# Performance work log

Measured on AMD Instinct MI355X. Metric: run time of the kernel, lower is better.

Reference implementation:

```python
import jax, jax.numpy as jnp
import numpy as np

B, W, F_IN = 128, 128, 64   # batch, window_size, num_features
N = 64                      # nodes per graph == num_features == tcn_out_channels
E = 4096                    # edges per graph
ED = 16                     # edge_feature_dim
H, C = 4, 32                # heads, gat_out_dim
FLAT = N * H * C            # 8192
HID = FLAT // 4             # 2048
LRELU_SLOPE = 0.01          # F.leaky_relu default
BN_EPS = 1e-5


def setup_inputs() -> dict:
    key = jax.random.key(0)
    ks = jax.random.split(key, 16)
    x = jax.random.normal(ks[0], (B, W, F_IN), jnp.float32)
    edge_index = jax.random.randint(ks[1], (2, E), 0, N)
    edge_attr = jax.random.normal(ks[2], (B, E, ED), jnp.float32)
    s = lambda k, shape, fan: jax.random.normal(k, shape, jnp.float32) / np.sqrt(fan)
    tcn_w = s(ks[3], (N, F_IN, 3), F_IN * 3)
    tcn_b = jnp.zeros((N,), jnp.float32)
    lin_l_w = s(ks[4], (H * C, W), W)
    lin_l_b = jnp.zeros((H * C,), jnp.float32)
    lin_e_w = s(ks[5], (H * C, ED), ED)
    lin_e_b = jnp.zeros((H * C,), jnp.float32)
    att = s(ks[6], (1, H, C), C)
    fc1_w = s(ks[7], (HID, FLAT), FLAT)
    fc1_b = jnp.zeros((HID,), jnp.float32)
    bn_g = jnp.ones((HID,), jnp.float32)
    bn_b = jnp.zeros((HID,), jnp.float32)
    fc2_w = s(ks[8], (2, HID), HID)
    fc2_b = jnp.zeros((2,), jnp.float32)
    return dict(x=x, edge_index=edge_index, edge_attr=edge_attr,
                tcn_w=tcn_w, tcn_b=tcn_b,
                lin_l_w=lin_l_w, lin_l_b=lin_l_b,
                lin_e_w=lin_e_w, lin_e_b=lin_e_b, att=att,
                fc1_w=fc1_w, fc1_b=fc1_b, bn_g=bn_g, bn_b=bn_b,
                fc2_w=fc2_w, fc2_b=fc2_b)


def reference(x, edge_index, edge_attr, tcn_w, tcn_b,
              lin_l_w, lin_l_b, lin_e_w, lin_e_b, att,
              fc1_w, fc1_b, bn_g, bn_b, fc2_w, fc2_b):
    # TCN: Conv1d(k=3, pad=1) over the window dim
    xt = jnp.transpose(x, (0, 2, 1))  # [B, F_IN, W]
    x_g = jax.lax.conv_general_dilated(
        xt, tcn_w, window_strides=(1,), padding=((1, 1),),
        dimension_numbers=('NCH', 'OIH', 'NCH')) + tcn_b[None, :, None]
    # x_g: [B, N, W] -> per-sample graph with N nodes, W-dim node features

    src, dst = edge_index[0], edge_index[1]

    def gat_one(xn, ea):
        # xn: [N, W], ea: [E, ED]
        h = (xn @ lin_l_w.T + lin_l_b).reshape(N, H, C)
        e = (ea @ lin_e_w.T + lin_e_b).reshape(E, H, C)
        xi = h[dst]               # [E, H, C] target node feats
        xj = h[src]               # [E, H, C] source node feats
        a = jax.nn.leaky_relu(xi + xj + e, LRELU_SLOPE)
        score = jnp.einsum('ehc,ohc->eh', a, att)  # [E, H]
        # segment softmax over edges grouped by destination node
        m = jax.ops.segment_max(score, dst, num_segments=N)
        m = jnp.where(jnp.isfinite(m), m, 0.0)
        ex = jnp.exp(score - m[dst])
        den = jax.ops.segment_sum(ex, dst, num_segments=N)
        alpha = ex / (den[dst] + 1e-16)            # [E, H]
        msg = xj * alpha[:, :, None]               # [E, H, C]
        out = jax.ops.segment_sum(msg, dst, num_segments=N)  # [N, H, C]
        return out.reshape(N, H * C)

    x_gat = jax.vmap(gat_one)(x_g, edge_attr)      # [B, N, H*C]
    x_gat = jax.nn.elu(x_gat)
    x_flat = x_gat.reshape(B, FLAT)

    h1 = x_flat @ fc1_w.T + fc1_b
    # BatchNorm1d in eval mode with fresh running stats (mean=0, var=1)
    h1 = h1 * (bn_g / jnp.sqrt(1.0 + BN_EPS)) + bn_b
    h1 = jax.nn.relu(h1)  # dropout is identity in eval
    logits = h1 @ fc2_w.T + fc2_b
    return logits
```

## Files before the change

### kernel.cpp

```cpp
#include <hip/hip_runtime.h>
#include <math.h>

#define BB   128
#define WW   128
#define FIN  64
#define NNODE 64
#define NE   4096
#define EDIM 16
#define NH   4
#define CDIM 32
#define HC   128
#define FLATD 8192
#define HIDD 2048

#define OFF_H    0u
#define OFF_P    1048576u
#define OFF_XGB  3211264u
#define OFF_BK   4259840u

typedef unsigned short u16;
typedef u16    u16x8  __attribute__((ext_vector_type(8)));
typedef u16    u16x4  __attribute__((ext_vector_type(4)));
typedef __bf16 bf16x8 __attribute__((ext_vector_type(8)));
typedef float  f32x4  __attribute__((ext_vector_type(4)));
typedef float  f32x16 __attribute__((ext_vector_type(16)));

__device__ __forceinline__ u16 f2bf(float f) {
    unsigned u = __float_as_uint(f);
    u += 0x7fffu + ((u >> 16) & 1u);
    return (u16)(u >> 16);
}
__device__ __forceinline__ void hilo(float v, u16* h, u16* l) {
    u16 hh = f2bf(v);
    float hf = __uint_as_float(((unsigned)hh) << 16);
    *h = hh;
    *l = f2bf(v - hf);
}

__global__ __launch_bounds__(256) void k0_bucket(
        const int* __restrict__ ei, int* __restrict__ bstart, int* __restrict__ blist)
{
    __shared__ int cnt[64];
    __shared__ int cur[65];
    const int t = threadIdx.x;
    if (t < 64) cnt[t] = 0;
    __syncthreads();
    for (int e = t; e < NE; e += 256) atomicAdd(&cnt[ei[NE + e]], 1);
    __syncthreads();
    if (t == 0) {
        int run = 0;
        for (int n = 0; n < 64; ++n) { cur[n] = run; run += cnt[n]; }
        cur[64] = run;
    }
    __syncthreads();
    if (t < 65) bstart[t] = cur[t];
    __syncthreads();
    for (int e = t; e < NE; e += 256) {
        int d = ei[NE + e], s = ei[e];
        int p = atomicAdd(&cur[d], 1);
        blist[p] = (e << 12) | (d << 6) | s;
    }
}

__global__ __launch_bounds__(256) void k1_tcn_linl(
        const float* __restrict__ x, const float* __restrict__ tcn_w,
        const float* __restrict__ tcn_b, const float* __restrict__ lin_l_w,
        const float* __restrict__ lin_l_b, float* __restrict__ h)
{
    __shared__ float xs[130*65];
    __shared__ float xg[32*132];
    const int b = blockIdx.x, half = blockIdx.y, t = threadIdx.x;
    const int n0 = half * 32;

    for (int idx = t; idx < 8192; idx += 256) {
        int w = idx >> 6, i = idx & 63;
        xs[(w+1)*65 + i] = x[b*8192 + idx];
    }
    if (t < 65) { xs[t] = 0.f; xs[129*65 + t] = 0.f; }
    __syncthreads();

    {
        const int nl = t >> 3;
        const int n  = n0 + nl;
        const int w0 = (t & 7) * 16;
        float acc[16];
        const float tb = tcn_b[n];
#pragma unroll
        for (int j = 0; j < 16; ++j) acc[j] = tb;
        for (int i = 0; i < 64; ++i) {
            const float t0 = tcn_w[n*192 + 3*i + 0];
            const float t1 = tcn_w[n*192 + 3*i + 1];
            const float t2 = tcn_w[n*192 + 3*i + 2];
            float a = xs[(w0+0)*65 + i];
            float c0 = xs[(w0+1)*65 + i];
#pragma unroll
            for (int dw = 0; dw < 16; ++dw) {
                float c = xs[(w0+dw+2)*65 + i];
                acc[dw] += a*t0 + c0*t1 + c*t2;
                a = c0; c0 = c;
            }
        }
#pragma unroll
        for (int dw = 0; dw < 16; ++dw) xg[nl*132 + w0 + dw] = acc[dw];
    }
    __syncthreads();

    {
        const int o2 = t & 63, ng = t >> 6;
        const int oA = o2, oB = o2 + 64;
        float accA[8], accB[8];
        const float lbA = lin_l_b[oA], lbB = lin_l_b[oB];
#pragma unroll
        for (int j = 0; j < 8; ++j) { accA[j] = lbA; accB[j] = lbB; }
        for (int c = 0; c < 32; ++c) {
            const float4 lwA = *(const float4*)&lin_l_w[oA*128 + c*4];
            const float4 lwB = *(const float4*)&lin_l_w[oB*128 + c*4];
#pragma unroll
            for (int nn = 0; nn < 8; ++nn) {
                const float4 xv = *(const float4*)&xg[(ng*8+nn)*132 + c*4];
                accA[nn] += xv.x*lwA.x + xv.y*lwA.y + xv.z*lwA.z + xv.w*lwA.w;
                accB[nn] += xv.x*lwB.x + xv.y*lwB.y + xv.z*lwB.z + xv.w*lwB.w;
            }
        }
#pragma unroll
        for (int nn = 0; nn < 8; ++nn) {
            const int n = n0 + ng*8 + nn;
            h[(b*64 + n)*128 + oA] = accA[nn];
            h[(b*64 + n)*128 + oB] = accB[nn];
        }
    }
}

#define CAPF 1600
__global__ __launch_bounds__(512, 2) void k2_fused(
        const float* __restrict__ hbase, const float* __restrict__ ea,
        const float* __restrict__ lin_e_w, const float* __restrict__ lin_e_b,
        const float* __restrict__ att, const int* __restrict__ bstart,
        const int* __restrict__ blist, u16* __restrict__ xgb)
{
    __shared__ float hbuf[64*132];
    __shared__ float scl[CAPF*4];
    __shared__ float Pm[4][16][68];
    __shared__ int   bst[17];
    const int b = blockIdx.x, quart = blockIdx.y, t = threadIdx.x;
    const int lane = t & 63, wv = t >> 6, l32 = lane & 31, h5 = lane >> 5;

    for (int idx = t; idx < 2048; idx += 512) {
        const int row = idx >> 5, c4 = (idx & 31) * 4;
        float4 hv = *(const float4*)&hbase[(size_t)b*8192 + row*128 + c4];
        const float4 eb = *(const float4*)&lin_e_b[c4];
        hv.x += 0.5f*eb.x; hv.y += 0.5f*eb.y;
        hv.z += 0.5f*eb.z; hv.w += 0.5f*eb.w;
        *(float4*)&hbuf[row*132 + c4] = hv;
    }
    {
        const f32x4 z4 = {0.f, 0.f, 0.f, 0.f};
        for (int idx = t; idx < 4*16*68/4; idx += 512) ((f32x4*)Pm)[idx] = z4;
    }
    if (t < 17) bst[t] = bstart[quart*16 + t];
    bf16x8 Ah[4], Al[4];
#pragma unroll
    for (int mt = 0; mt < 4; ++mt) {
        const float* wp = &lin_e_w[(mt*32 + l32)*16 + h5*8];
        const float4 w0 = *(const float4*)wp;
        const float4 w1 = *(const float4*)(wp + 4);
        u16 th[8], tl[8];
        hilo(w0.x,&th[0],&tl[0]); hilo(w0.y,&th[1],&tl[1]);
        hilo(w0.z,&th[2],&tl[2]); hilo(w0.w,&th[3],&tl[3]);
        hilo(w1.x,&th[4],&tl[4]); hilo(w1.y,&th[5],&tl[5]);
        hilo(w1.z,&th[6],&tl[6]); hilo(w1.w,&th[7],&tl[7]);
        u16x8 vh = { th[0],th[1],th[2],th[3],th[4],th[5],th[6],th[7] };
        u16x8 vl = { tl[0],tl[1],tl[2],tl[3],tl[4],tl[5],tl[6],tl[7] };
        Ah[mt] = *(bf16x8*)&vh;
        Al[mt] = *(bf16x8*)&vl;
    }
    float4 attv[4][4];
#pragma unroll
    for (int mt = 0; mt < 4; ++mt)
#pragma unroll
        for (int g = 0; g < 4; ++g)
            attv[mt][g] = *(const float4*)&att[mt*32 + g*8 + h5*4];
    __syncthreads();

    const int lo = bst[0], cnt = min(bst[16] - lo, CAPF);
    const int gcnt = (cnt + 31) >> 5;

    for (int g = wv; g < gcnt; g += 8) {
        const int idx = g*32 + l32;
        const bool valid = idx < cnt;
        const int pk = valid ? blist[lo + idx] : 0;
        const int sn = pk & 63, dd = (pk >> 6) & 63, e = pk >> 12;
        const float* eap = ea + ((size_t)b*NE + e)*16 + h5*8;
        const float4 v0 = *(const float4*)eap;
        const float4 v1 = *(const float4*)(eap + 4);
        u16 bh[8], bl[8];
        hilo(v0.x,&bh[0],&bl[0]); hilo(v0.y,&bh[1],&bl[1]);
        hilo(v0.z,&bh[2],&bl[2]); hilo(v0.w,&bh[3],&bl[3]);
        hilo(v1.x,&bh[4],&bl[4]); hilo(v1.y,&bh[5],&bl[5]);
        hilo(v1.z,&bh[6],&bl[6]); hilo(v1.w,&bh[7],&bl[7]);
        u16x8 vbh = { bh[0],bh[1],bh[2],bh[3],bh[4],bh[5],bh[6],bh[7] };
        u16x8 vbl = { bl[0],bl[1],bl[2],bl[3],bl[4],bl[5],bl[6],bl[7] };
        const bf16x8 Bh = *(bf16x8*)&vbh;
        const bf16x8 Bl = *(bf16x8*)&vbl;
        float hacc[4];
#pragma unroll
        for (int mt = 0; mt < 4; ++mt) {
            f32x16 D = {0.f,0.f,0.f,0.f,0.f,0.f,0.f,0.f,
                        0.f,0.f,0.f,0.f,0.f,0.f,0.f,0.f};
            D = __builtin_amdgcn_mfma_f32_32x32x16_bf16(Al[mt], Bh, D, 0, 0, 0);
            D = __builtin_amdgcn_mfma_f32_32x32x16_bf16(Ah[mt], Bl, D, 0, 0, 0);
            D = __builtin_amdgcn_mfma_f32_32x32x16_bf16(Ah[mt], Bh, D, 0, 0, 0);
            float s = 0.f;
#pragma unroll
            for (int g4 = 0; g4 < 4; ++g4) {
                const int ob = mt*32 + g4*8 + h5*4;
                const float4 hd = *(const float4*)&hbuf[dd*132 + ob];
                const float4 hs = *(const float4*)&hbuf[sn*132 + ob];
                float x0 = hd.x + hs.x + D[g4*4+0];
                float x1 = hd.y + hs.y + D[g4*4+1];
                float x2 = hd.z + hs.z + D[g4*4+2];
                float x3 = hd.w + hs.w + D[g4*4+3];
                x0 = fmaxf(x0, 0.01f*x0); x1 = fmaxf(x1, 0.01f*x1);
                x2 = fmaxf(x2, 0.01f*x2); x3 = fmaxf(x3, 0.01f*x3);
                const float4 a4 = attv[mt][g4];
                s += a4.x*x0 + a4.y*x1 + a4.z*x2 + a4.w*x3;
            }
            hacc[mt] = s;
        }
#pragma unroll
        for (int hh = 0; hh < 4; ++hh)
            hacc[hh] += __shfl_xor(hacc[hh], 32);
        if (h5 == 0 && valid)
            *(float4*)&scl[idx*4] = make_float4(hacc[0], hacc[1], hacc[2], hacc[3]);
    }
    __syncthreads();

    {
        const int pair = t >> 3, sub = t & 7;
        const int nl = pair >> 2, hh = pair & 3;
        const int s0 = bst[nl] - lo, s1 = bst[nl+1] - lo;
        float mx = -3.4e38f;
        for (int i = s0 + sub; i < s1; i += 8) mx = fmaxf(mx, scl[i*4 + hh]);
        mx = fmaxf(mx, __shfl_xor(mx, 1));
        mx = fmaxf(mx, __shfl_xor(mx, 2));
        mx = fmaxf(mx, __shfl_xor(mx, 4));
        float den = 0.f;
        for (int i = s0 + sub; i < s1; i += 8) {
            const float ex = __expf(scl[i*4 + hh] - mx);
            scl[i*4 + hh] = ex;
            den += ex;
        }
        den += __shfl_xor(den, 1);
        den += __shfl_xor(den, 2);
        den += __shfl_xor(den, 4);
        const float rd = 1.0f / (den + 1e-16f);
        for (int i = s0 + sub; i < s1; i += 8) {
            const int src = blist[lo + i] & 63;
            atomicAdd(&Pm[hh][nl][src], scl[i*4 + hh] * rd);
        }
    }
    __syncthreads();

    {
        const int hh = wv >> 1, ct = wv & 1;
        const int l16 = lane & 15, q = lane >> 4;
        const int cb = hh*32 + ct*16 + l16;
        f32x4 D = {0.f, 0.f, 0.f, 0.f};
#pragma unroll
        for (int k0 = 0; k0 < 64; k0 += 32) {
            const float* pp = &Pm[hh][l16][k0 + q*8];
            const float4 a0 = *(const float4*)pp;
            const float4 a1 = *(const float4*)(pp + 4);
            u16 ph[8], pl[8];
            hilo(a0.x,&ph[0],&pl[0]); hilo(a0.y,&ph[1],&pl[1]);
            hilo(a0.z,&ph[2],&pl[2]); hilo(a0.w,&ph[3],&pl[3]);
            hilo(a1.x,&ph[4],&pl[4]); hilo(a1.y,&ph[5],&pl[5]);
            hilo(a1.z,&ph[6],&pl[6]); hilo(a1.w,&ph[7],&pl[7]);
            u16x8 vph = { ph[0],ph[1],ph[2],ph[3],ph[4],ph[5],ph[6],ph[7] };
            u16x8 vpl = { pl[0],pl[1],pl[2],pl[3],pl[4],pl[5],pl[6],pl[7] };
            u16 hhv[8], hlv[8];
#pragma unroll
            for (int i = 0; i < 8; ++i) {
                const float v = hbuf[(k0 + q*8 + i)*132 + cb];
                hilo(v, &hhv[i], &hlv[i]);
            }
            u16x8 vhh = { hhv[0],hhv[1],hhv[2],hhv[3],hhv[4],hhv[5],hhv[6],hhv[7] };
            u16x8 vhl = { hlv[0],hlv[1],hlv[2],hlv[3],hlv[4],hlv[5],hlv[6],hlv[7] };
            const bf16x8 Ph = *(bf16x8*)&vph, Pl = *(bf16x8*)&vpl;
            const bf16x8 Hh = *(bf16x8*)&vhh, Hl = *(bf16x8*)&vhl;
            D = __builtin_amdgcn_mfma_f32_16x16x32_bf16(Pl, Hh, D, 0, 0, 0);
            D = __builtin_amdgcn_mfma_f32_16x16x32_bf16(Ph, Hl, D, 0, 0, 0);
            D = __builtin_amdgcn_mfma_f32_16x16x32_bf16(Ph, Hh, D, 0, 0, 0);
        }
        const float lb2 = 0.5f * lin_e_b[cb];
#pragma unroll
        for (int r = 0; r < 4; ++r) {
            const int m = q*4 + r;
            const float corr = (bst[m+1] > bst[m]) ? lb2 : 0.f;
            float v = D[r] - corr;
            v = v > 0.f ? v : expm1f(v);
            xgb[(size_t)b*8192 + (quart*16 + m)*128 + cb] = f2bf(v);
        }
    }
}

__global__ __launch_bounds__(256) void k3_fc1(
        const u16* __restrict__ xgb, const float* __restrict__ fc1_w,
        float* __restrict__ part)
{
    __shared__ u16 Ash[128*72];
    __shared__ u16 Bsh[32*72];
    const int jb = blockIdx.x, ks = blockIdx.y, t = threadIdx.x;
    const int j0 = jb*32, k0 = ks*1024;
    const int wave = t >> 6, lane = t & 63;
    const int quad = lane >> 4, l16 = lane & 15;
    const int wm = (wave & 1) * 64, wn = (wave >> 1) * 16;

    f32x4 acc[4];
#pragma unroll
    for (int i = 0; i < 4; ++i) acc[i] = (f32x4){0.f, 0.f, 0.f, 0.f};

    const int arow = t >> 1, acol = (t & 1) * 32;
    const int brow = t >> 3, bcol = (t & 7) * 8;

    for (int kc = 0; kc < 1024; kc += 64) {
        if (kc) __syncthreads();
        const u16* ap = xgb + (size_t)arow*FLATD + k0 + kc + acol;
#pragma unroll
        for (int qq = 0; qq < 4; ++qq)
            *(u16x8*)&Ash[arow*72 + acol + qq*8] = *(const u16x8*)(ap + qq*8);
        const float* bp = fc1_w + (size_t)(j0 + brow)*FLATD + k0 + kc + bcol;
        {
            float4 v0 = *(const float4*)(bp);
            float4 v1 = *(const float4*)(bp + 4);
            u16x8 u = { f2bf(v0.x), f2bf(v0.y), f2bf(v0.z), f2bf(v0.w),
                        f2bf(v1.x), f2bf(v1.y), f2bf(v1.z), f2bf(v1.w) };
            *(u16x8*)&Bsh[brow*72 + bcol] = u;
        }
        __syncthreads();
#pragma unroll
        for (int kk = 0; kk < 64; kk += 32) {
            bf16x8 af[4], bfr;
#pragma unroll
            for (int i = 0; i < 4; ++i)
                af[i] = *(const bf16x8*)&Ash[(wm + i*16 + l16)*72 + kk + quad*8];
            bfr = *(const bf16x8*)&Bsh[(wn + l16)*72 + kk + quad*8];
#pragma unroll
            for (int i = 0; i < 4; ++i)
                acc[i] = __builtin_amdgcn_mfma_f32_16x16x32_bf16(af[i], bfr, acc[i], 0, 0, 0);
        }
    }
#pragma unroll
    for (int i = 0; i < 4; ++i) {
        const int n = j0 + wn + l16;
#pragma unroll
        for (int r = 0; r < 4; ++r) {
            const int m = wm + i*16 + quad*4 + r;
            part[(size_t)ks*262144 + (size_t)m*HIDD + n] = acc[i][r];
        }
    }
}

__global__ __launch_bounds__(256) void k4_fc2(
        const float* __restrict__ part, const float* __restrict__ fc1_b,
        const float* __restrict__ bn_g, const float* __restrict__ bn_b,
        const float* __restrict__ fc2_w, const float* __restrict__ fc2_b,
        float* __restrict__ out)
{
    __shared__ float r0[256], r1[256];
    const int b = blockIdx.x, t = threadIdx.x;
    const float inv = 1.0f / sqrtf(1.0f + 1e-5f);
    float p0 = 0.f, p1 = 0.f;
    for (int j = t; j < 2048; j += 256) {
        float hv = 0.f;
#pragma unroll
        for (int s = 0; s < 8; ++s) hv += part[(size_t)s*262144 + (size_t)b*2048 + j];
        float v = (hv + fc1_b[j]) * (bn_g[j] * inv) + bn_b[j];
        v = fmaxf(v, 0.f);
        p0 += v * fc2_w[j];
        p1 += v * fc2_w[2048 + j];
    }
    r0[t] = p0; r1[t] = p1;
    __syncthreads();
    for (int s = 128; s > 0; s >>= 1) {
        if (t < s) { r0[t] += r0[t+s]; r1[t] += r1[t+s]; }
        __syncthreads();
    }
    if (t == 0) {
        out[b*2 + 0] = r0[0] + fc2_b[0];
        out[b*2 + 1] = r1[0] + fc2_b[1];
    }
}

extern "C" void kernel_launch(void* const* d_in, const int* in_sizes, int n_in,
                              void* d_out, int out_size, void* d_ws, size_t ws_size,
                              hipStream_t stream)
{
    const float* x       = (const float*)d_in[0];
    const int*   ei      = (const int*)  d_in[1];
    const float* ea      = (const float*)d_in[2];
    const float* tcn_w   = (const float*)d_in[3];
    const float* tcn_b   = (const float*)d_in[4];
    const float* lin_l_w = (const float*)d_in[5];
    const float* lin_l_b = (const float*)d_in[6];
    const float* lin_e_w = (const float*)d_in[7];
    const float* lin_e_b = (const float*)d_in[8];
    const float* att     = (const float*)d_in[9];
    const float* fc1_w   = (const float*)d_in[10];
    const float* fc1_b   = (const float*)d_in[11];
    const float* bn_g    = (const float*)d_in[12];
    const float* bn_b    = (const float*)d_in[13];
    const float* fc2_w   = (const float*)d_in[14];
    const float* fc2_b   = (const float*)d_in[15];

    float* ws     = (float*)d_ws;
    float* hbuf   = ws + OFF_H;
    float* part   = ws + OFF_P;
    u16*   xgb    = (u16*)(ws + OFF_XGB);
    int*   bstart = (int*)(ws + OFF_BK);
    int*   blist  = bstart + 80;
    float* out    = (float*)d_out;

    k0_bucket  <<<1, 256, 0, stream>>>(ei, bstart, blist);
    k1_tcn_linl<<<dim3(BB, 2), 256, 0, stream>>>(x, tcn_w, tcn_b, lin_l_w, lin_l_b, hbuf);
    k2_fused   <<<dim3(BB, 4), 512, 0, stream>>>(hbuf, ea, lin_e_w, lin_e_b, att,
                                                 bstart, blist, xgb);
    k3_fc1     <<<dim3(64, 8), 256, 0, stream>>>(xgb, fc1_w, part);
    k4_fc2     <<<BB, 256, 0, stream>>>(part, fc1_b, bn_g, bn_b, fc2_w, fc2_b, out);
}
```

Measured before the change: 252.1 us.

## Merge bucket and TCN kernels, halve GAT split, prefetch edge and fc1 loads

The bucketing kernel is folded into the TCN/lin_l launch as an extra block, and the TCN weights are staged in shared memory. The GAT kernel now handles 32 destination nodes per block instead of 16, with a larger edge-score buffer and occupancy dropped to one block per CU. It also software-prefetches the next edge group's index and features, and reuses the H fragments across two M tiles. The fc1 GEMM register-prefetches the next K slice before the MFMA loop. Together these aim to cut launch count and hide global-load latency, at the cost of fewer, larger GAT blocks (256 total) and more shared-memory pressure.

```diff
diff --git a/kernel.cpp b/kernel.cpp
--- a/kernel.cpp
+++ b/kernel.cpp
@@ -37,44 +37,52 @@
     *l = f2bf(v - hf);
 }
 
-__global__ __launch_bounds__(256) void k0_bucket(
-        const int* __restrict__ ei, int* __restrict__ bstart, int* __restrict__ blist)
-{
-    __shared__ int cnt[64];
-    __shared__ int cur[65];
-    const int t = threadIdx.x;
-    if (t < 64) cnt[t] = 0;
-    __syncthreads();
-    for (int e = t; e < NE; e += 256) atomicAdd(&cnt[ei[NE + e]], 1);
-    __syncthreads();
-    if (t == 0) {
-        int run = 0;
-        for (int n = 0; n < 64; ++n) { cur[n] = run; run += cnt[n]; }
-        cur[64] = run;
-    }
-    __syncthreads();
-    if (t < 65) bstart[t] = cur[t];
-    __syncthreads();
-    for (int e = t; e < NE; e += 256) {
-        int d = ei[NE + e], s = ei[e];
-        int p = atomicAdd(&cur[d], 1);
-        blist[p] = (e << 12) | (d << 6) | s;
-    }
-}
-
-__global__ __launch_bounds__(256) void k1_tcn_linl(
+__global__ __launch_bounds__(256) void k01(
         const float* __restrict__ x, const float* __restrict__ tcn_w,
         const float* __restrict__ tcn_b, const float* __restrict__ lin_l_w,
-        const float* __restrict__ lin_l_b, float* __restrict__ h)
+        const float* __restrict__ lin_l_b, float* __restrict__ h,
+        const int* __restrict__ ei, int* __restrict__ bstart,
+        int* __restrict__ blist)
 {
     __shared__ float xs[130*65];
     __shared__ float xg[32*132];
-    const int b = blockIdx.x, half = blockIdx.y, t = threadIdx.x;
+    __shared__ float tw[32*192];
+    __shared__ int cnt[64];
+    __shared__ int cur[65];
+    const int bid = blockIdx.x, t = threadIdx.x;
+
+    if (bid == 256) {
+        if (t < 64) cnt[t] = 0;
+        __syncthreads();
+        for (int e = t; e < NE; e += 256) atomicAdd(&cnt[ei[NE + e]], 1);
+        __syncthreads();
+        if (t == 0) {
+            int run = 0;
+            for (int n = 0; n < 64; ++n) { cur[n] = run; run += cnt[n]; }
+            cur[64] = run;
+        }
+        __syncthreads();
+        if (t < 65) bstart[t] = cur[t];
+        __syncthreads();
+        for (int e = t; e < NE; e += 256) {
+            int d = ei[NE + e], s = ei[e];
+            int p = atomicAdd(&cur[d], 1);
+            blist[p] = (e << 12) | (d << 6) | s;
+        }
+        return;
+    }
+
+    const int b = bid >> 1, half = bid & 1;
     const int n0 = half * 32;
 
     for (int idx = t; idx < 8192; idx += 256) {
         int w = idx >> 6, i = idx & 63;
         xs[(w+1)*65 + i] = x[b*8192 + idx];
+    }
+    {
+        const float4* src = (const float4*)(tcn_w + n0*192);
+        for (int idx = t; idx < 1536; idx += 256)
+            ((float4*)tw)[idx] = src[idx];
     }
     if (t < 65) { xs[t] = 0.f; xs[129*65 + t] = 0.f; }
     __syncthreads();
@@ -88,9 +96,9 @@
 #pragma unroll
         for (int j = 0; j < 16; ++j) acc[j] = tb;
         for (int i = 0; i < 64; ++i) {
-            const float t0 = tcn_w[n*192 + 3*i + 0];
-            const float t1 = tcn_w[n*192 + 3*i + 1];
-            const float t2 = tcn_w[n*192 + 3*i + 2];
+            const float t0 = tw[nl*192 + 3*i + 0];
+            const float t1 = tw[nl*192 + 3*i + 1];
+            const float t2 = tw[nl*192 + 3*i + 2];
             float a = xs[(w0+0)*65 + i];
             float c0 = xs[(w0+1)*65 + i];
 #pragma unroll
@@ -131,8 +139,8 @@
     }
 }
 
-#define CAPF 1600
-__global__ __launch_bounds__(512, 2) void k2_fused(
+#define CAPF 2560
+__global__ __launch_bounds__(512, 1) void k2_fused(
         const float* __restrict__ hbase, const float* __restrict__ ea,
         const float* __restrict__ lin_e_w, const float* __restrict__ lin_e_b,
         const float* __restrict__ att, const int* __restrict__ bstart,
@@ -140,10 +148,26 @@
 {
     __shared__ float hbuf[64*132];
     __shared__ float scl[CAPF*4];
-    __shared__ float Pm[4][16][68];
-    __shared__ int   bst[17];
-    const int b = blockIdx.x, quart = blockIdx.y, t = threadIdx.x;
+    __shared__ float Pm[4][32][68];
+    __shared__ int   bst[33];
+    const int b = blockIdx.x, half = blockIdx.y, t = threadIdx.x;
     const int lane = t & 63, wv = t >> 6, l32 = lane & 31, h5 = lane >> 5;
+
+    const int lo  = bstart[half*32];
+    const int cnt = min(bstart[half*32 + 32] - lo, CAPF);
+    const int gcnt = (cnt + 31) >> 5;
+
+    int g = wv;
+    int pkc = 0; bool validc = false;
+    float4 v0c = {0.f,0.f,0.f,0.f}, v1c = {0.f,0.f,0.f,0.f};
+    if (g < gcnt) {
+        const int idx0 = g*32 + l32;
+        validc = idx0 < cnt;
+        pkc = validc ? blist[lo + idx0] : 0;
+        const float* eap = ea + ((size_t)b*NE + (size_t)(pkc >> 12))*16 + h5*8;
+        v0c = *(const float4*)eap;
+        v1c = *(const float4*)(eap + 4);
+    }
 
     for (int idx = t; idx < 2048; idx += 512) {
         const int row = idx >> 5, c4 = (idx & 31) * 4;
@@ -155,9 +179,9 @@
     }
     {
         const f32x4 z4 = {0.f, 0.f, 0.f, 0.f};
-        for (int idx = t; idx < 4*16*68/4; idx += 512) ((f32x4*)Pm)[idx] = z4;
-    }
-    if (t < 17) bst[t] = bstart[quart*16 + t];
+        for (int idx = t; idx < 4*32*68/4; idx += 512) ((f32x4*)Pm)[idx] = z4;
+    }
+    if (t < 33) bst[t] = bstart[half*32 + t];
     bf16x8 Ah[4], Al[4];
 #pragma unroll
     for (int mt = 0; mt < 4; ++mt) {
@@ -178,21 +202,26 @@
 #pragma unroll
     for (int mt = 0; mt < 4; ++mt)
 #pragma unroll
-        for (int g = 0; g < 4; ++g)
-            attv[mt][g] = *(const float4*)&att[mt*32 + g*8 + h5*4];
-    __syncthreads();
-
-    const int lo = bst[0], cnt = min(bst[16] - lo, CAPF);
-    const int gcnt = (cnt + 31) >> 5;
-
-    for (int g = wv; g < gcnt; g += 8) {
+        for (int gq = 0; gq < 4; ++gq)
+            attv[mt][gq] = *(const float4*)&att[mt*32 + gq*8 + h5*4];
+    __syncthreads();
+
+    while (g < gcnt) {
+        const int gn = g + 8;
+        const int pk = pkc; const bool valid = validc;
+        const float4 v0 = v0c, v1 = v1c;
         const int idx = g*32 + l32;
-        const bool valid = idx < cnt;
-        const int pk = valid ? blist[lo + idx] : 0;
-        const int sn = pk & 63, dd = (pk >> 6) & 63, e = pk >> 12;
-        const float* eap = ea + ((size_t)b*NE + e)*16 + h5*8;
-        const float4 v0 = *(const float4*)eap;
-        const float4 v1 = *(const float4*)(eap + 4);
+        if (gn < gcnt) {
+            const int idxn = gn*32 + l32;
+            validc = idxn < cnt;
+            pkc = validc ? blist[lo + idxn] : 0;
+            const float* eap = ea + ((size_t)b*NE + (size_t)(pkc >> 12))*16 + h5*8;
+            v0c = *(const float4*)eap;
+            v1c = *(const float4*)(eap + 4);
+        } else {
+            validc = false;
+        }
+        const int sn = pk & 63, dd = (pk >> 6) & 63;
         u16 bh[8], bl[8];
         hilo(v0.x,&bh[0],&bl[0]); hilo(v0.y,&bh[1],&bl[1]);
         hilo(v0.z,&bh[2],&bl[2]); hilo(v0.w,&bh[3],&bl[3]);
@@ -232,29 +261,28 @@
             hacc[hh] += __shfl_xor(hacc[hh], 32);
         if (h5 == 0 && valid)
             *(float4*)&scl[idx*4] = make_float4(hacc[0], hacc[1], hacc[2], hacc[3]);
-    }
-    __syncthreads();
-
-    {
-        const int pair = t >> 3, sub = t & 7;
+        g = gn;
+    }
+    __syncthreads();
+
+    {
+        const int pair = t >> 2, sub = t & 3;
         const int nl = pair >> 2, hh = pair & 3;
         const int s0 = bst[nl] - lo, s1 = bst[nl+1] - lo;
         float mx = -3.4e38f;
-        for (int i = s0 + sub; i < s1; i += 8) mx = fmaxf(mx, scl[i*4 + hh]);
+        for (int i = s0 + sub; i < s1; i += 4) mx = fmaxf(mx, scl[i*4 + hh]);
         mx = fmaxf(mx, __shfl_xor(mx, 1));
         mx = fmaxf(mx, __shfl_xor(mx, 2));
-        mx = fmaxf(mx, __shfl_xor(mx, 4));
         float den = 0.f;
-        for (int i = s0 + sub; i < s1; i += 8) {
+        for (int i = s0 + sub; i < s1; i += 4) {
             const float ex = __expf(scl[i*4 + hh] - mx);
             scl[i*4 + hh] = ex;
             den += ex;
         }
         den += __shfl_xor(den, 1);
         den += __shfl_xor(den, 2);
-        den += __shfl_xor(den, 4);
         const float rd = 1.0f / (den + 1e-16f);
-        for (int i = s0 + sub; i < s1; i += 8) {
+        for (int i = s0 + sub; i < s1; i += 4) {
             const int src = blist[lo + i] & 63;
             atomicAdd(&Pm[hh][nl][src], scl[i*4 + hh] * rd);
         }
@@ -265,41 +293,49 @@
         const int hh = wv >> 1, ct = wv & 1;
         const int l16 = lane & 15, q = lane >> 4;
         const int cb = hh*32 + ct*16 + l16;
-        f32x4 D = {0.f, 0.f, 0.f, 0.f};
-#pragma unroll
-        for (int k0 = 0; k0 < 64; k0 += 32) {
-            const float* pp = &Pm[hh][l16][k0 + q*8];
-            const float4 a0 = *(const float4*)pp;
-            const float4 a1 = *(const float4*)(pp + 4);
-            u16 ph[8], pl[8];
-            hilo(a0.x,&ph[0],&pl[0]); hilo(a0.y,&ph[1],&pl[1]);
-            hilo(a0.z,&ph[2],&pl[2]); hilo(a0.w,&ph[3],&pl[3]);
-            hilo(a1.x,&ph[4],&pl[4]); hilo(a1.y,&ph[5],&pl[5]);
-            hilo(a1.z,&ph[6],&pl[6]); hilo(a1.w,&ph[7],&pl[7]);
-            u16x8 vph = { ph[0],ph[1],ph[2],ph[3],ph[4],ph[5],ph[6],ph[7] };
-            u16x8 vpl = { pl[0],pl[1],pl[2],pl[3],pl[4],pl[5],pl[6],pl[7] };
+        const float lb2 = 0.5f * lin_e_b[cb];
+        bf16x8 Hh2[2], Hl2[2];
+#pragma unroll
+        for (int kk = 0; kk < 2; ++kk) {
             u16 hhv[8], hlv[8];
 #pragma unroll
             for (int i = 0; i < 8; ++i) {
-                const float v = hbuf[(k0 + q*8 + i)*132 + cb];
+                const float v = hbuf[(kk*32 + q*8 + i)*132 + cb];
                 hilo(v, &hhv[i], &hlv[i]);
             }
             u16x8 vhh = { hhv[0],hhv[1],hhv[2],hhv[3],hhv[4],hhv[5],hhv[6],hhv[7] };
             u16x8 vhl = { hlv[0],hlv[1],hlv[2],hlv[3],hlv[4],hlv[5],hlv[6],hlv[7] };
-            const bf16x8 Ph = *(bf16x8*)&vph, Pl = *(bf16x8*)&vpl;
-            const bf16x8 Hh = *(bf16x8*)&vhh, Hl = *(bf16x8*)&vhl;
-            D = __builtin_amdgcn_mfma_f32_16x16x32_bf16(Pl, Hh, D, 0, 0, 0);
-            D = __builtin_amdgcn_mfma_f32_16x16x32_bf16(Ph, Hl, D, 0, 0, 0);
-            D = __builtin_amdgcn_mfma_f32_16x16x32_bf16(Ph, Hh, D, 0, 0, 0);
-        }
-        const float lb2 = 0.5f * lin_e_b[cb];
-#pragma unroll
-        for (int r = 0; r < 4; ++r) {
-            const int m = q*4 + r;
-            const float corr = (bst[m+1] > bst[m]) ? lb2 : 0.f;
-            float v = D[r] - corr;
-            v = v > 0.f ? v : expm1f(v);
-            xgb[(size_t)b*8192 + (quart*16 + m)*128 + cb] = f2bf(v);
+            Hh2[kk] = *(bf16x8*)&vhh;
+            Hl2[kk] = *(bf16x8*)&vhl;
+        }
+#pragma unroll
+        for (int mrow = 0; mrow < 32; mrow += 16) {
+            f32x4 D = {0.f, 0.f, 0.f, 0.f};
+#pragma unroll
+            for (int kk = 0; kk < 2; ++kk) {
+                const float* pp = &Pm[hh][mrow + l16][kk*32 + q*8];
+                const float4 a0 = *(const float4*)pp;
+                const float4 a1 = *(const float4*)(pp + 4);
+                u16 ph[8], pl[8];
+                hilo(a0.x,&ph[0],&pl[0]); hilo(a0.y,&ph[1],&pl[1]);
+                hilo(a0.z,&ph[2],&pl[2]); hilo(a0.w,&ph[3],&pl[3]);
+                hilo(a1.x,&ph[4],&pl[4]); hilo(a1.y,&ph[5],&pl[5]);
+                hilo(a1.z,&ph[6],&pl[6]); hilo(a1.w,&ph[7],&pl[7]);
+                u16x8 vph = { ph[0],ph[1],ph[2],ph[3],ph[4],ph[5],ph[6],ph[7] };
+                u16x8 vpl = { pl[0],pl[1],pl[2],pl[3],pl[4],pl[5],pl[6],pl[7] };
+                const bf16x8 Ph = *(bf16x8*)&vph, Pl = *(bf16x8*)&vpl;
+                D = __builtin_amdgcn_mfma_f32_16x16x32_bf16(Pl, Hh2[kk], D, 0, 0, 0);
+                D = __builtin_amdgcn_mfma_f32_16x16x32_bf16(Ph, Hl2[kk], D, 0, 0, 0);
+                D = __builtin_amdgcn_mfma_f32_16x16x32_bf16(Ph, Hh2[kk], D, 0, 0, 0);
+            }
+#pragma unroll
+            for (int r = 0; r < 4; ++r) {
+                const int m = mrow + q*4 + r;
+                const float corr = (bst[m+1] > bst[m]) ? lb2 : 0.f;
+                float v = D[r] - corr;
+                v = v > 0.f ? v : expm1f(v);
+                xgb[(size_t)b*8192 + (half*32 + m)*128 + cb] = f2bf(v);
+            }
         }
     }
 }
@@ -323,21 +359,32 @@
     const int arow = t >> 1, acol = (t & 1) * 32;
     const int brow = t >> 3, bcol = (t & 7) * 8;
 
+    u16x8 Ar[4]; float4 Br0, Br1;
+    {
+        const u16* ap = xgb + (size_t)arow*FLATD + k0 + acol;
+#pragma unroll
+        for (int qq = 0; qq < 4; ++qq) Ar[qq] = *(const u16x8*)(ap + qq*8);
+        const float* bp = fc1_w + (size_t)(j0 + brow)*FLATD + k0 + bcol;
+        Br0 = *(const float4*)bp; Br1 = *(const float4*)(bp + 4);
+    }
+
     for (int kc = 0; kc < 1024; kc += 64) {
-        if (kc) __syncthreads();
-        const u16* ap = xgb + (size_t)arow*FLATD + k0 + kc + acol;
 #pragma unroll
         for (int qq = 0; qq < 4; ++qq)
-            *(u16x8*)&Ash[arow*72 + acol + qq*8] = *(const u16x8*)(ap + qq*8);
-        const float* bp = fc1_w + (size_t)(j0 + brow)*FLATD + k0 + kc + bcol;
+            *(u16x8*)&Ash[arow*72 + acol + qq*8] = Ar[qq];
         {
-            float4 v0 = *(const float4*)(bp);
-            float4 v1 = *(const float4*)(bp + 4);
-            u16x8 u = { f2bf(v0.x), f2bf(v0.y), f2bf(v0.z), f2bf(v0.w),
-                        f2bf(v1.x), f2bf(v1.y), f2bf(v1.z), f2bf(v1.w) };
+            u16x8 u = { f2bf(Br0.x), f2bf(Br0.y), f2bf(Br0.z), f2bf(Br0.w),
+                        f2bf(Br1.x), f2bf(Br1.y), f2bf(Br1.z), f2bf(Br1.w) };
             *(u16x8*)&Bsh[brow*72 + bcol] = u;
         }
         __syncthreads();
+        if (kc + 64 < 1024) {
+            const u16* ap = xgb + (size_t)arow*FLATD + k0 + kc + 64 + acol;
+#pragma unroll
+            for (int qq = 0; qq < 4; ++qq) Ar[qq] = *(const u16x8*)(ap + qq*8);
+            const float* bp = fc1_w + (size_t)(j0 + brow)*FLATD + k0 + kc + 64 + bcol;
+            Br0 = *(const float4*)bp; Br1 = *(const float4*)(bp + 4);
+        }
 #pragma unroll
         for (int kk = 0; kk < 64; kk += 32) {
             bf16x8 af[4], bfr;
@@ -349,6 +396,7 @@
             for (int i = 0; i < 4; ++i)
                 acc[i] = __builtin_amdgcn_mfma_f32_16x16x32_bf16(af[i], bfr, acc[i], 0, 0, 0);
         }
+        __syncthreads();
     }
 #pragma unroll
     for (int i = 0; i < 4; ++i) {
@@ -421,10 +469,10 @@
     int*   blist  = bstart + 80;
     float* out    = (float*)d_out;
 
-    k0_bucket  <<<1, 256, 0, stream>>>(ei, bstart, blist);
-    k1_tcn_linl<<<dim3(BB, 2), 256, 0, stream>>>(x, tcn_w, tcn_b, lin_l_w, lin_l_b, hbuf);
-    k2_fused   <<<dim3(BB, 4), 512, 0, stream>>>(hbuf, ea, lin_e_w, lin_e_b, att,
-                                                 bstart, blist, xgb);
-    k3_fc1     <<<dim3(64, 8), 256, 0, stream>>>(xgb, fc1_w, part);
-    k4_fc2     <<<BB, 256, 0, stream>>>(part, fc1_b, bn_g, bn_b, fc2_w, fc2_b, out);
-}
+    k01    <<<257, 256, 0, stream>>>(x, tcn_w, tcn_b, lin_l_w, lin_l_b, hbuf,
+                                     ei, bstart, blist);
+    k2_fused<<<dim3(BB, 2), 512, 0, stream>>>(hbuf, ea, lin_e_w, lin_e_b, att,
+                                              bstart, blist, xgb);
+    k3_fc1 <<<dim3(64, 8), 256, 0, stream>>>(xgb, fc1_w, part);
+    k4_fc2 <<<BB, 256, 0, stream>>>(part, fc1_b, bn_g, bn_b, fc2_w, fc2_b, out);
+}
```

After: 233.4 us. 7.4% less time.
